# Performance work log

Measured on AMD Instinct MI355X. Metric: run time of the kernel, lower is better.

## Reference

```python
import jax, jax.numpy as jnp
import numpy as np

N = 50000    # nodes
E = 600000   # edges
F = 128      # num_features
ED = 16      # edge_dim
H = 4        # heads
D = 32       # per-head channels = hidden_units // heads
HID = H * D  # hidden_units = 128
C = 10       # num_classes


def _lin(k, fan_in, fan_out):
    # torch.nn.Linear-style init scale
    return jax.random.uniform(k, (fan_in, fan_out), jnp.float32, -1.0, 1.0) / np.sqrt(fan_in)


def setup_inputs() -> dict:
    key = jax.random.key(0)
    ks = jax.random.split(key, 24)
    inp = {
        "x": jax.random.normal(ks[0], (N, F), jnp.float32),
        "edge_index": jax.random.randint(ks[1], (2, E), 0, N, dtype=jnp.int32),
        "edge_attr": jax.random.normal(ks[2], (E, ED), jnp.float32),
    }
    j = 3
    for l, ind in enumerate([F, HID]):
        specs = {"q": (ind, HID, True), "k": (ind, HID, True), "v": (ind, HID, True),
                 "e": (ED, HID, False), "s": (ind, HID, True)}
        for nm, (i, o, bias) in specs.items():
            inp[f"W{nm}{l}"] = _lin(ks[j], i, o); j += 1
            if bias:
                inp[f"b{nm}{l}"] = jnp.zeros((o,), jnp.float32)
    inp["Wout"] = _lin(ks[j], HID, C)
    inp["bout"] = jnp.zeros((C,), jnp.float32)
    return inp


def _transformer_conv(x, src, dst, eattr, Wq, bq, Wk, bk, Wv, bv, We, Ws, bs):
    # PyG TransformerConv: concat=True, root_weight=True, beta=False, eval dropout.
    n = x.shape[0]
    q = (x @ Wq + bq).reshape(n, H, D)
    k = (x @ Wk + bk).reshape(n, H, D)
    v = (x @ Wv + bv).reshape(n, H, D)
    e = (eattr @ We).reshape(-1, H, D)           # edge embedding, added to key and value
    kj = k[src] + e                              # [E, H, D]
    vj = v[src] + e                              # [E, H, D]
    logits = jnp.einsum("ehd,ehd->eh", q[dst], kj) / np.sqrt(D)
    m = jax.ops.segment_max(logits, dst, num_segments=n)          # [N, H]
    ex = jnp.exp(logits - m[dst])
    denom = jax.ops.segment_sum(ex, dst, num_segments=n)          # [N, H]
    alpha = ex / (denom[dst] + 1e-16)                             # PyG softmax eps
    out = jax.ops.segment_sum(vj * alpha[..., None], dst, num_segments=n)
    return out.reshape(n, HID) + x @ Ws + bs                      # concat heads + skip


def reference(x, edge_index, edge_attr,
              Wq0, bq0, Wk0, bk0, Wv0, bv0, We0, Ws0, bs0,
              Wq1, bq1, Wk1, bk1, Wv1, bv1, We1, Ws1, bs1,
              Wout, bout):
    src, dst = edge_index[0], edge_index[1]
    h = jax.nn.relu(_transformer_conv(x, src, dst, edge_attr,
                                      Wq0, bq0, Wk0, bk0, Wv0, bv0, We0, Ws0, bs0))
    h = jax.nn.relu(_transformer_conv(h, src, dst, edge_attr,
                                      Wq1, bq1, Wk1, bk1, Wv1, bv1, We1, Ws1, bs1))
    logits = h @ Wout + bout
    return jax.nn.log_softmax(logits, axis=1)
```

## Files before the change

### kernel.cpp

```cpp
#include <hip/hip_runtime.h>

typedef unsigned short u16;
typedef unsigned int u32;
typedef __attribute__((ext_vector_type(4))) u16 u16x4;
typedef __attribute__((ext_vector_type(8))) u16 u16x8;
typedef __attribute__((ext_vector_type(4))) u32 u32x4;
typedef __attribute__((ext_vector_type(8))) short short8;
typedef __attribute__((ext_vector_type(4))) float f32x4;
typedef __attribute__((ext_vector_type(4))) float f4;

#define NN 50000
#define NE 600000
#define HEADS 4
#define DH 32
#define HIDU 128
#define NC 10
#define NBLK 196
#define WES_T 34
#define WES_H 546

__device__ __forceinline__ float bf2f(u16 u) {
    union { unsigned int i; float f; } c; c.i = ((unsigned int)u) << 16; return c.f;
}
__device__ __forceinline__ u16 f2bf(float f) {
    union { float f; unsigned int i; } c; c.f = f;
    unsigned int x = c.i;
    return (u16)((x + 0x7fffu + ((x >> 16) & 1u)) >> 16);
}
__device__ __forceinline__ float lo_bf(u32 d) { return __uint_as_float(d << 16); }
__device__ __forceinline__ float hi_bf(u32 d) { return __uint_as_float(d & 0xffff0000u); }
__device__ __forceinline__ float qadd_xor1(float v) {
    int o = __builtin_amdgcn_update_dpp(0, __float_as_int(v), 0xB1, 0xF, 0xF, true);
    return v + __int_as_float(o);
}
__device__ __forceinline__ float qadd_xor2(float v) {
    int o = __builtin_amdgcn_update_dpp(0, __float_as_int(v), 0x4E, 0xF, 0xF, true);
    return v + __int_as_float(o);
}

__global__ void k_zero(int* p, int n) {
    int i = blockIdx.x * blockDim.x + threadIdx.x;
    if (i < n) p[i] = 0;
}

__global__ void k_hist(const int* __restrict__ dst, int* __restrict__ deg) {
    int i = blockIdx.x * blockDim.x + threadIdx.x;
    if (i < NE) atomicAdd(&deg[dst[i]], 1);
}

__global__ __launch_bounds__(256) void scan_a(const int* __restrict__ deg,
                                              int* __restrict__ bsum) {
    __shared__ int red[4];
    int i = blockIdx.x * 256 + threadIdx.x;
    int v = (i < NN) ? deg[i] : 0;
    #pragma unroll
    for (int off = 1; off < 64; off <<= 1) v += __shfl_xor(v, off);
    if ((threadIdx.x & 63) == 0) red[threadIdx.x >> 6] = v;
    __syncthreads();
    if (threadIdx.x == 0) bsum[blockIdx.x] = red[0] + red[1] + red[2] + red[3];
}

__global__ __launch_bounds__(256) void scan_b(const int* __restrict__ bsum,
                                              int* __restrict__ boff,
                                              int* __restrict__ row_ptr) {
    __shared__ int s[256];
    int t = threadIdx.x;
    int v = (t < NBLK) ? bsum[t] : 0;
    s[t] = v;
    __syncthreads();
    for (int off = 1; off < 256; off <<= 1) {
        int x = (t >= off) ? s[t - off] : 0;
        __syncthreads();
        s[t] += x;
        __syncthreads();
    }
    if (t < NBLK) boff[t] = s[t] - v;
    if (t == 0) row_ptr[NN] = NE;
}

__global__ __launch_bounds__(256) void scan_c(const int* __restrict__ deg,
                                              const int* __restrict__ boff,
                                              int* __restrict__ row_ptr,
                                              int* __restrict__ cursor) {
    __shared__ int s[256];
    int t = threadIdx.x;
    int i = blockIdx.x * 256 + t;
    int v = (i < NN) ? deg[i] : 0;
    s[t] = v;
    __syncthreads();
    for (int off = 1; off < 256; off <<= 1) {
        int x = (t >= off) ? s[t - off] : 0;
        __syncthreads();
        s[t] += x;
        __syncthreads();
    }
    if (i < NN) {
        int r = boff[blockIdx.x] + s[t] - v;
        row_ptr[i] = r;
        cursor[i] = r;
    }
}

__global__ void k_scatter(const int* __restrict__ ei, const float* __restrict__ eattr,
                          int* __restrict__ cursor,
                          int* __restrict__ csr_src, u16* __restrict__ ea16) {
    int i = blockIdx.x * blockDim.x + threadIdx.x;
    if (i < NE) {
        int s = ei[i];
        int d = ei[NE + i];
        int pos = atomicAdd(&cursor[d], 1);
        csr_src[pos] = s;
        const f4* ep = (const f4*)(eattr + (size_t)i * 16);
        f4 a = ep[0], b = ep[1], c = ep[2], dd = ep[3];
        u16x8 o0, o1;
        #pragma unroll
        for (int j = 0; j < 4; j++) {
            o0[j] = f2bf(a[j]); o0[4 + j] = f2bf(b[j]);
            o1[j] = f2bf(c[j]); o1[4 + j] = f2bf(dd[j]);
        }
        *(u16x8*)(ea16 + (size_t)pos * 16)     = o0;
        *(u16x8*)(ea16 + (size_t)pos * 16 + 8) = o1;
    }
}

__global__ void k_cvtw(const float* w0, const float* w1, const float* w2, const float* w3,
                       const float* w4, const float* w5, const float* w6, const float* w7,
                       u16* __restrict__ hi) {
    const float* w;
    switch (blockIdx.x) {
        case 0: w = w0; break; case 1: w = w1; break;
        case 2: w = w2; break; case 3: w = w3; break;
        case 4: w = w4; break; case 5: w = w5; break;
        case 6: w = w6; break; default: w = w7; break;
    }
    u16* oh = hi + blockIdx.x * 16384;
    for (int i = 0; i < 64; i++) {
        int idx = threadIdx.x + i * 256;
        int k = idx >> 7, n = idx & 127;
        oh[n * 128 + k] = f2bf(w[idx]);
    }
}

__global__ __launch_bounds__(256) void gemm_qkvs(
    const float* __restrict__ X, const u16* __restrict__ WtHi,
    const float* __restrict__ b0, const float* __restrict__ b1,
    const float* __restrict__ b2, const float* __restrict__ b3,
    float* __restrict__ outq, u16* __restrict__ outk, u16* __restrict__ outv,
    float* __restrict__ outs, int nrows)
{
    __shared__ u16 Bs[128 * 128];
    const int mat = blockIdx.y;
    const u16* wh = WtHi + mat * 16384;

    #pragma unroll
    for (int i = 0; i < 8; i++) {
        int idx = threadIdx.x + i * 256;
        int n = idx >> 4, g = idx & 15;
        *(u16x8*)(&Bs[n * 128 + ((g ^ (n & 15)) << 3)]) = *(const u16x8*)(wh + n * 128 + g * 8);
    }
    __syncthreads();

    const int wave = threadIdx.x >> 6, lane = threadIdx.x & 63;
    const int n0 = lane & 15;
    const int qw = lane >> 4;
    const int kq = qw * 8;

    const float* xp[2];
    #pragma unroll
    for (int rt = 0; rt < 2; rt++) {
        int arow = blockIdx.x * 128 + wave * 32 + rt * 16 + n0;
        int arow_c = arow < nrows ? arow : nrows - 1;
        xp[rt] = X + (size_t)arow_c * HIDU + kq;
    }

    f32x4 acc[2][8];
    #pragma unroll
    for (int rt = 0; rt < 2; rt++)
        #pragma unroll
        for (int nt = 0; nt < 8; nt++) acc[rt][nt] = (f32x4){0.f, 0.f, 0.f, 0.f};

    #pragma unroll
    for (int ks = 0; ks < 4; ks++) {
        short8 ah[2];
        #pragma unroll
        for (int rt = 0; rt < 2; rt++) {
            f4 a0 = *(const f4*)(xp[rt] + ks * 32);
            f4 a1 = *(const f4*)(xp[rt] + ks * 32 + 4);
            #pragma unroll
            for (int j = 0; j < 4; j++) {
                ah[rt][j]     = (short)(__float_as_uint(a0[j]) >> 16);
                ah[rt][4 + j] = (short)(__float_as_uint(a1[j]) >> 16);
            }
        }
        #pragma unroll
        for (int nt = 0; nt < 8; nt++) {
            const int boff = (nt * 16 + n0) * 128 + (((ks << 2) + qw) ^ n0) * 8;
            short8 bh = *(const short8*)(&Bs[boff]);
            #pragma unroll
            for (int rt = 0; rt < 2; rt++)
                acc[rt][nt] = __builtin_amdgcn_mfma_f32_16x16x32_bf16(ah[rt], bh, acc[rt][nt], 0, 0, 0);
        }
    }

    const float* bia = (mat == 0) ? b0 : (mat == 1) ? b1 : (mat == 2) ? b2 : b3;
    #pragma unroll
    for (int rt = 0; rt < 2; rt++) {
        const int rbase = blockIdx.x * 128 + wave * 32 + rt * 16 + qw * 4;
        #pragma unroll
        for (int nt = 0; nt < 8; nt++) {
            int col = nt * 16 + n0;
            float bv = bia[col];
            #pragma unroll
            for (int r = 0; r < 4; r++) {
                int grow = rbase + r;
                if (grow < nrows) {
                    float v = acc[rt][nt][r] + bv;
                    if (mat == 0)      outq[(size_t)grow * HIDU + col] = v;
                    else if (mat == 1) outk[(size_t)grow * HIDU + col] = f2bf(v);
                    else if (mat == 2) outv[(size_t)grow * HIDU + col] = f2bf(v);
                    else               outs[(size_t)grow * HIDU + col] = v;
                }
            }
        }
    }
}

__global__ __launch_bounds__(256) void attn(
    const float* __restrict__ qb, const u16* __restrict__ kb, const u16* __restrict__ vb,
    const float* __restrict__ sb, const u16* __restrict__ ea16, const float* __restrict__ We,
    const int* __restrict__ row_ptr, const int* __restrict__ csr_src,
    float* __restrict__ hout_f32,
    const float* __restrict__ Wout, const float* __restrict__ bout,
    float* __restrict__ out_logits, int mode)
{
    __shared__ float WeS[4 * WES_H];
    __shared__ float WoS[HIDU * NC];
    __shared__ float boS[NC];
    __shared__ float hrowS[16 * 132];
    __shared__ float lgS[16 * 16];

    #pragma unroll
    for (int i = 0; i < 8; i++) {
        int idx = threadIdx.x + i * 256;
        int tt = idx >> 7, c = idx & 127;
        int h = c >> 5, j = c & 31;
        WeS[h * WES_H + tt * WES_T + j] = We[idx];
    }
    if (mode == 1) {
        for (int i = 0; i < 5; i++) {
            int idx = threadIdx.x + i * 256;
            if (idx < HIDU * NC) WoS[idx] = Wout[idx];
        }
        if (threadIdx.x < NC) boS[threadIdx.x] = bout[threadIdx.x];
    }
    __syncthreads();

    int gtid = blockIdx.x * 256 + threadIdx.x;
    int n   = gtid >> 4;
    int l16 = gtid & 15;
    int h   = l16 >> 2;
    int sub = l16 & 3;
    const int lane = threadIdx.x & 63;
    const float* WeH = &WeS[h * WES_H];
    const int j0  = sub * 8;
    const int ch0 = h * DH + j0;
    const int t0  = sub * 4;

    f4 qa, qbv;
    float g4[4];
    {
        const f4* qp = (const f4*)(qb + (size_t)n * HIDU + h * DH);
        float q32[32];
        #pragma unroll
        for (int c = 0; c < 8; c++) {
            f4 x = qp[c];
            #pragma unroll
            for (int j = 0; j < 4; j++) q32[c * 4 + j] = x[j];
        }
        #pragma unroll
        for (int tt = 0; tt < 4; tt++) {
            float a = 0.f;
            #pragma unroll
            for (int j = 0; j < 32; j++) a += q32[j] * WeH[(t0 + tt) * WES_T + j];
            g4[tt] = a;
        }
        #pragma unroll
        for (int j = 0; j < 4; j++) { qa[j] = q32[j0 + j]; qbv[j] = q32[j0 + 4 + j]; }
    }

    float m = -INFINITY, l = 0.f;
    f4 O0 = {0.f, 0.f, 0.f, 0.f}, O1 = {0.f, 0.f, 0.f, 0.f};
    f4 a4 = {0.f, 0.f, 0.f, 0.f};

    const int r0 = row_ptr[n], r1 = row_ptr[n + 1];
    const float inv = 0.17677669529663687f;

    for (int e = r0; e < r1; e += 2) {
        bool has2 = (e + 1 < r1);
        int e1i = has2 ? e + 1 : e;
        int s0 = csr_src[e];
        int s1 = csr_src[e1i];
        u16x4 e0 = *(const u16x4*)(ea16 + (size_t)e * 16 + t0);
        u16x4 e1 = *(const u16x4*)(ea16 + (size_t)e1i * 16 + t0);

        u32x4 k0 = *(const u32x4*)(kb + (size_t)s0 * HIDU + ch0);
        u32x4 v0 = *(const u32x4*)(vb + (size_t)s0 * HIDU + ch0);
        u32x4 k1 = *(const u32x4*)(kb + (size_t)s1 * HIDU + ch0);
        u32x4 v1 = *(const u32x4*)(vb + (size_t)s1 * HIDU + ch0);

        f4 k0a = {lo_bf(k0[0]), hi_bf(k0[0]), lo_bf(k0[1]), hi_bf(k0[1])};
        f4 k0b = {lo_bf(k0[2]), hi_bf(k0[2]), lo_bf(k0[3]), hi_bf(k0[3])};
        f4 k1a = {lo_bf(k1[0]), hi_bf(k1[0]), lo_bf(k1[1]), hi_bf(k1[1])};
        f4 k1b = {lo_bf(k1[2]), hi_bf(k1[2]), lo_bf(k1[3]), hi_bf(k1[3])};
        f4 ea0 = {bf2f(e0[0]), bf2f(e0[1]), bf2f(e0[2]), bf2f(e0[3])};
        f4 ea1 = {bf2f(e1[0]), bf2f(e1[1]), bf2f(e1[2]), bf2f(e1[3])};
        f4 g4v = {g4[0], g4[1], g4[2], g4[3]};

        f4 acc0 = qa * k0a + qbv * k0b + g4v * ea0;
        f4 acc1 = qa * k1a + qbv * k1b + g4v * ea1;
        float d0 = acc0[0] + acc0[1] + acc0[2] + acc0[3];
        float d1 = acc1[0] + acc1[1] + acc1[2] + acc1[3];
        d0 = qadd_xor1(d0);  d1 = qadd_xor1(d1);
        d0 = qadd_xor2(d0);  d1 = qadd_xor2(d1);

        float logit0 = d0 * inv;
        float logit1 = has2 ? d1 * inv : -INFINITY;
        float mn = fmaxf(m, fmaxf(logit0, logit1));
        float corr = __expf(m - mn);
        float w0 = __expf(logit0 - mn);
        float w1 = __expf(logit1 - mn);
        l = l * corr + w0 + w1;

        f4 v0a = {lo_bf(v0[0]), hi_bf(v0[0]), lo_bf(v0[1]), hi_bf(v0[1])};
        f4 v0b = {lo_bf(v0[2]), hi_bf(v0[2]), lo_bf(v0[3]), hi_bf(v0[3])};
        f4 v1a = {lo_bf(v1[0]), hi_bf(v1[0]), lo_bf(v1[1]), hi_bf(v1[1])};
        f4 v1b = {lo_bf(v1[2]), hi_bf(v1[2]), lo_bf(v1[3]), hi_bf(v1[3])};
        O0 = O0 * corr + v0a * w0 + v1a * w1;
        O1 = O1 * corr + v0b * w0 + v1b * w1;
        a4 = a4 * corr + ea0 * w0 + ea1 * w1;
        m = mn;
    }

    float af[16];
    #pragma unroll
    for (int t = 0; t < 16; t++)
        af[t] = __shfl(a4[t & 3], (lane & ~3) | (t >> 2));

    float invl = 1.0f / (l + 1e-16f);
    const float* sp = sb + (size_t)n * HIDU + ch0;

    float vals[8];
    #pragma unroll
    for (int j = 0; j < 8; j++) {
        float ev = 0.f;
        #pragma unroll
        for (int t = 0; t < 16; t++) ev += af[t] * WeH[t * WES_T + j0 + j];
        float Oj = (j < 4) ? O0[j] : O1[j - 4];
        vals[j] = fmaxf((Oj + ev) * invl + sp[j], 0.f);
    }

    if (mode == 0) {
        const size_t obase = (size_t)n * HIDU + ch0;
        f4 r0v, r1v;
        #pragma unroll
        for (int j = 0; j < 4; j++) { r0v[j] = vals[j]; r1v[j] = vals[4 + j]; }
        *(f4*)(hout_f32 + obase) = r0v;
        *(f4*)(hout_f32 + obase + 4) = r1v;
    } else {
        const int cb = threadIdx.x >> 4;
        float* hr = &hrowS[cb * 132];
        f4 w0v, w1v;
        #pragma unroll
        for (int j = 0; j < 4; j++) { w0v[j] = vals[j]; w1v[j] = vals[4 + j]; }
        *(f4*)(hr + ch0) = w0v;
        *(f4*)(hr + ch0 + 4) = w1v;
        if (l16 < NC) {
            float lg = boS[l16];
            for (int ch = 0; ch < HIDU; ch += 4) {
                f4 hv = *(const f4*)(hr + ch);
                #pragma unroll
                for (int j = 0; j < 4; j++) lg += hv[j] * WoS[(ch + j) * NC + l16];
            }
            lgS[cb * 16 + l16] = lg;
        }
        if (l16 < NC) {
            float lgc = lgS[cb * 16 + l16];
            float mx = -INFINITY;
            #pragma unroll
            for (int c = 0; c < NC; c++) mx = fmaxf(mx, lgS[cb * 16 + c]);
            float sum = 0.f;
            #pragma unroll
            for (int c = 0; c < NC; c++) sum += __expf(lgS[cb * 16 + c] - mx);
            float lse = mx + __logf(sum);
            out_logits[(size_t)n * NC + l16] = lgc - lse;
        }
    }
}

extern "C" void kernel_launch(void* const* d_in, const int* in_sizes, int n_in,
                              void* d_out, int out_size, void* d_ws, size_t ws_size,
                              hipStream_t stream) {
    const float* x     = (const float*)d_in[0];
    const int*   ei    = (const int*)d_in[1];
    const float* eattr = (const float*)d_in[2];
    const float *Wq0 = (const float*)d_in[3],  *bq0 = (const float*)d_in[4];
    const float *Wk0 = (const float*)d_in[5],  *bk0 = (const float*)d_in[6];
    const float *Wv0 = (const float*)d_in[7],  *bv0 = (const float*)d_in[8];
    const float *We0 = (const float*)d_in[9];
    const float *Ws0 = (const float*)d_in[10], *bs0 = (const float*)d_in[11];
    const float *Wq1 = (const float*)d_in[12], *bq1 = (const float*)d_in[13];
    const float *Wk1 = (const float*)d_in[14], *bk1 = (const float*)d_in[15];
    const float *Wv1 = (const float*)d_in[16], *bv1 = (const float*)d_in[17];
    const float *We1 = (const float*)d_in[18];
    const float *Ws1 = (const float*)d_in[19], *bs1 = (const float*)d_in[20];
    const float *Wout = (const float*)d_in[21], *bout = (const float*)d_in[22];

    char* p = (char*)d_ws;
    auto alloc = [&](size_t bytes) -> void* {
        void* r = (void*)p;
        p += (bytes + 255) & ~(size_t)255;
        return r;
    };
    int* deg      = (int*)alloc(NN * 4);
    int* row_ptr  = (int*)alloc((NN + 1) * 4);
    int* cursor   = (int*)alloc(NN * 4);
    int* bsum     = (int*)alloc(NBLK * 4);
    int* boff     = (int*)alloc(NBLK * 4);
    int* csr_src  = (int*)alloc((size_t)NE * 4);
    float* qb     = (float*)alloc((size_t)NN * HIDU * 4);
    u16* kb       = (u16*)alloc((size_t)NN * HIDU * 2);
    u16* vb       = (u16*)alloc((size_t)NN * HIDU * 2);
    float* sbuf   = (float*)alloc((size_t)NN * HIDU * 4);
    float* hbuf   = (float*)alloc((size_t)NN * HIDU * 4);
    u16* ea16     = (u16*)alloc((size_t)NE * 16 * 2);
    u16* wthi     = (u16*)alloc(8 * 16384 * 2);

    k_zero<<<(NN + 255) / 256, 256, 0, stream>>>(deg, NN);
    k_hist<<<(NE + 255) / 256, 256, 0, stream>>>(ei + NE, deg);
    scan_a<<<NBLK, 256, 0, stream>>>(deg, bsum);
    scan_b<<<1, 256, 0, stream>>>(bsum, boff, row_ptr);
    scan_c<<<NBLK, 256, 0, stream>>>(deg, boff, row_ptr, cursor);
    k_scatter<<<(NE + 255) / 256, 256, 0, stream>>>(ei, eattr, cursor, csr_src, ea16);

    k_cvtw<<<8, 256, 0, stream>>>(Wq0, Wk0, Wv0, Ws0, Wq1, Wk1, Wv1, Ws1, wthi);

    const int gm = (NN + 127) / 128;
    const int ga = (NN * 16) / 256;

    gemm_qkvs<<<dim3(gm, 4), 256, 0, stream>>>(x, wthi, bq0, bk0, bv0, bs0,
                                               qb, kb, vb, sbuf, NN);
    attn<<<ga, 256, 0, stream>>>(qb, kb, vb, sbuf, ea16, We0, row_ptr, csr_src,
                                 hbuf, Wout, bout, (float*)d_out, 0);
    gemm_qkvs<<<dim3(gm, 4), 256, 0, stream>>>(hbuf, wthi + 4 * 16384, bq1, bk1, bv1, bs1,
                                               qb, kb, vb, sbuf, NN);
    attn<<<ga, 256, 0, stream>>>(qb, kb, vb, sbuf, ea16, We1, row_ptr, csr_src,
                                 hbuf, Wout, bout, (float*)d_out, 1);
}
```

Before: 452.8 us.

## Unroll attention edge loop by four, templatize mode, shuffle-reduce output projection

Templates the attention kernel on mode so shared buffers and branches for the unused path vanish. It processes four edges per online-softmax step instead of two, using exp2 with a prescaled logit constant. The q·We projection is now split across the 4 lanes of a head and combined with DPP reductions, replacing a 32-wide per-lane loop. The final classifier is computed by all 16 lanes with a transposed Wout in shared memory and xor-shuffle reductions, removing the LDS staging of hidden rows. More loads in flight per iteration should hide gather latency, at the cost of extra registers and wasted duplicate loads on nodes with few edges.

Result: faster. 433.1 us (-4.4%).

```diff
diff --git a/kernel.cpp b/kernel.cpp
--- a/kernel.cpp
+++ b/kernel.cpp
@@ -8,6 +8,7 @@
 typedef __attribute__((ext_vector_type(8))) short short8;
 typedef __attribute__((ext_vector_type(4))) float f32x4;
 typedef __attribute__((ext_vector_type(4))) float f4;
+typedef __attribute__((ext_vector_type(2))) float f2;
 
 #define NN 50000
 #define NE 600000
@@ -18,6 +19,8 @@
 #define NBLK 196
 #define WES_T 34
 #define WES_H 546
+
+#define SCALE2 0.25503486164f
 
 __device__ __forceinline__ float bf2f(u16 u) {
     union { unsigned int i; float f; } c; c.i = ((unsigned int)u) << 16; return c.f;
@@ -225,19 +228,18 @@
     }
 }
 
-__global__ __launch_bounds__(256) void attn(
+template<int MODE>
+__global__ __launch_bounds__(256) void attn_t(
     const float* __restrict__ qb, const u16* __restrict__ kb, const u16* __restrict__ vb,
     const float* __restrict__ sb, const u16* __restrict__ ea16, const float* __restrict__ We,
     const int* __restrict__ row_ptr, const int* __restrict__ csr_src,
     float* __restrict__ hout_f32,
     const float* __restrict__ Wout, const float* __restrict__ bout,
-    float* __restrict__ out_logits, int mode)
+    float* __restrict__ out_logits)
 {
     __shared__ float WeS[4 * WES_H];
-    __shared__ float WoS[HIDU * NC];
-    __shared__ float boS[NC];
-    __shared__ float hrowS[16 * 132];
-    __shared__ float lgS[16 * 16];
+    __shared__ float WoT[MODE ? (NC * HIDU) : 1];
+    __shared__ float boS[MODE ? NC : 1];
 
     #pragma unroll
     for (int i = 0; i < 8; i++) {
@@ -246,10 +248,14 @@
         int h = c >> 5, j = c & 31;
         WeS[h * WES_H + tt * WES_T + j] = We[idx];
     }
-    if (mode == 1) {
+    if (MODE == 1) {
+        #pragma unroll
         for (int i = 0; i < 5; i++) {
             int idx = threadIdx.x + i * 256;
-            if (idx < HIDU * NC) WoS[idx] = Wout[idx];
+            if (idx < HIDU * NC) {
+                int c = idx >> 7, ch = idx & 127;
+                WoT[idx] = Wout[ch * NC + c];
+            }
         }
         if (threadIdx.x < NC) boS[threadIdx.x] = bout[threadIdx.x];
     }
@@ -267,25 +273,24 @@
     const int t0  = sub * 4;
 
     f4 qa, qbv;
-    float g4[4];
     {
-        const f4* qp = (const f4*)(qb + (size_t)n * HIDU + h * DH);
-        float q32[32];
-        #pragma unroll
-        for (int c = 0; c < 8; c++) {
-            f4 x = qp[c];
-            #pragma unroll
-            for (int j = 0; j < 4; j++) q32[c * 4 + j] = x[j];
-        }
-        #pragma unroll
-        for (int tt = 0; tt < 4; tt++) {
-            float a = 0.f;
-            #pragma unroll
-            for (int j = 0; j < 32; j++) a += q32[j] * WeH[(t0 + tt) * WES_T + j];
-            g4[tt] = a;
-        }
-        #pragma unroll
-        for (int j = 0; j < 4; j++) { qa[j] = q32[j0 + j]; qbv[j] = q32[j0 + 4 + j]; }
+        const f4* qp = (const f4*)(qb + (size_t)n * HIDU + ch0);
+        qa = qp[0]; qbv = qp[1];
+    }
+
+    f4 g4v;
+    {
+        float part[16];
+        #pragma unroll
+        for (int t = 0; t < 16; t++) {
+            const f2* wp = (const f2*)(WeH + t * WES_T + j0);
+            f2 w0 = wp[0], w1 = wp[1], w2 = wp[2], w3 = wp[3];
+            part[t] = qa[0] * w0.x + qa[1] * w0.y + qa[2] * w1.x + qa[3] * w1.y
+                    + qbv[0] * w2.x + qbv[1] * w2.y + qbv[2] * w3.x + qbv[3] * w3.y;
+        }
+        #pragma unroll
+        for (int t = 0; t < 16; t++) { part[t] = qadd_xor1(part[t]); part[t] = qadd_xor2(part[t]); }
+        g4v[0] = part[t0]; g4v[1] = part[t0 + 1]; g4v[2] = part[t0 + 2]; g4v[3] = part[t0 + 3];
     }
 
     float m = -INFINITY, l = 0.f;
@@ -293,51 +298,73 @@
     f4 a4 = {0.f, 0.f, 0.f, 0.f};
 
     const int r0 = row_ptr[n], r1 = row_ptr[n + 1];
-    const float inv = 0.17677669529663687f;
-
-    for (int e = r0; e < r1; e += 2) {
-        bool has2 = (e + 1 < r1);
-        int e1i = has2 ? e + 1 : e;
-        int s0 = csr_src[e];
-        int s1 = csr_src[e1i];
-        u16x4 e0 = *(const u16x4*)(ea16 + (size_t)e * 16 + t0);
-        u16x4 e1 = *(const u16x4*)(ea16 + (size_t)e1i * 16 + t0);
-
+
+    for (int e = r0; e < r1; e += 4) {
+        const int e1 = (e + 1 < r1) ? e + 1 : e;
+        const int e2 = (e + 2 < r1) ? e + 2 : e;
+        const int e3 = (e + 3 < r1) ? e + 3 : e;
+        int s0 = csr_src[e], s1 = csr_src[e1], s2 = csr_src[e2], s3 = csr_src[e3];
+        u16x4 x0 = *(const u16x4*)(ea16 + (size_t)e  * 16 + t0);
+        u16x4 x1 = *(const u16x4*)(ea16 + (size_t)e1 * 16 + t0);
+        u16x4 x2 = *(const u16x4*)(ea16 + (size_t)e2 * 16 + t0);
+        u16x4 x3 = *(const u16x4*)(ea16 + (size_t)e3 * 16 + t0);
         u32x4 k0 = *(const u32x4*)(kb + (size_t)s0 * HIDU + ch0);
+        u32x4 k1 = *(const u32x4*)(kb + (size_t)s1 * HIDU + ch0);
+        u32x4 k2 = *(const u32x4*)(kb + (size_t)s2 * HIDU + ch0);
+        u32x4 k3 = *(const u32x4*)(kb + (size_t)s3 * HIDU + ch0);
         u32x4 v0 = *(const u32x4*)(vb + (size_t)s0 * HIDU + ch0);
-        u32x4 k1 = *(const u32x4*)(kb + (size_t)s1 * HIDU + ch0);
         u32x4 v1 = *(const u32x4*)(vb + (size_t)s1 * HIDU + ch0);
-
-        f4 k0a = {lo_bf(k0[0]), hi_bf(k0[0]), lo_bf(k0[1]), hi_bf(k0[1])};
-        f4 k0b = {lo_bf(k0[2]), hi_bf(k0[2]), lo_bf(k0[3]), hi_bf(k0[3])};
-        f4 k1a = {lo_bf(k1[0]), hi_bf(k1[0]), lo_bf(k1[1]), hi_bf(k1[1])};
-        f4 k1b = {lo_bf(k1[2]), hi_bf(k1[2]), lo_bf(k1[3]), hi_bf(k1[3])};
-        f4 ea0 = {bf2f(e0[0]), bf2f(e0[1]), bf2f(e0[2]), bf2f(e0[3])};
-        f4 ea1 = {bf2f(e1[0]), bf2f(e1[1]), bf2f(e1[2]), bf2f(e1[3])};
-        f4 g4v = {g4[0], g4[1], g4[2], g4[3]};
-
-        f4 acc0 = qa * k0a + qbv * k0b + g4v * ea0;
-        f4 acc1 = qa * k1a + qbv * k1b + g4v * ea1;
-        float d0 = acc0[0] + acc0[1] + acc0[2] + acc0[3];
-        float d1 = acc1[0] + acc1[1] + acc1[2] + acc1[3];
-        d0 = qadd_xor1(d0);  d1 = qadd_xor1(d1);
-        d0 = qadd_xor2(d0);  d1 = qadd_xor2(d1);
-
-        float logit0 = d0 * inv;
-        float logit1 = has2 ? d1 * inv : -INFINITY;
-        float mn = fmaxf(m, fmaxf(logit0, logit1));
-        float corr = __expf(m - mn);
-        float w0 = __expf(logit0 - mn);
-        float w1 = __expf(logit1 - mn);
-        l = l * corr + w0 + w1;
-
-        f4 v0a = {lo_bf(v0[0]), hi_bf(v0[0]), lo_bf(v0[1]), hi_bf(v0[1])};
-        f4 v0b = {lo_bf(v0[2]), hi_bf(v0[2]), lo_bf(v0[3]), hi_bf(v0[3])};
-        f4 v1a = {lo_bf(v1[0]), hi_bf(v1[0]), lo_bf(v1[1]), hi_bf(v1[1])};
-        f4 v1b = {lo_bf(v1[2]), hi_bf(v1[2]), lo_bf(v1[3]), hi_bf(v1[3])};
-        O0 = O0 * corr + v0a * w0 + v1a * w1;
-        O1 = O1 * corr + v0b * w0 + v1b * w1;
-        a4 = a4 * corr + ea0 * w0 + ea1 * w1;
+        u32x4 v2 = *(const u32x4*)(vb + (size_t)s2 * HIDU + ch0);
+        u32x4 v3 = *(const u32x4*)(vb + (size_t)s3 * HIDU + ch0);
+
+        f4 ea0 = {bf2f(x0[0]), bf2f(x0[1]), bf2f(x0[2]), bf2f(x0[3])};
+        f4 ea1 = {bf2f(x1[0]), bf2f(x1[1]), bf2f(x1[2]), bf2f(x1[3])};
+        f4 ea2 = {bf2f(x2[0]), bf2f(x2[1]), bf2f(x2[2]), bf2f(x2[3])};
+        f4 ea3 = {bf2f(x3[0]), bf2f(x3[1]), bf2f(x3[2]), bf2f(x3[3])};
+
+        f4 ac0 = qa * (f4){lo_bf(k0[0]), hi_bf(k0[0]), lo_bf(k0[1]), hi_bf(k0[1])}
+               + qbv * (f4){lo_bf(k0[2]), hi_bf(k0[2]), lo_bf(k0[3]), hi_bf(k0[3])}
+               + g4v * ea0;
+        f4 ac1 = qa * (f4){lo_bf(k1[0]), hi_bf(k1[0]), lo_bf(k1[1]), hi_bf(k1[1])}
+               + qbv * (f4){lo_bf(k1[2]), hi_bf(k1[2]), lo_bf(k1[3]), hi_bf(k1[3])}
+               + g4v * ea1;
+        f4 ac2 = qa * (f4){lo_bf(k2[0]), hi_bf(k2[0]), lo_bf(k2[1]), hi_bf(k2[1])}
+               + qbv * (f4){lo_bf(k2[2]), hi_bf(k2[2]), lo_bf(k2[3]), hi_bf(k2[3])}
+               + g4v * ea2;
+        f4 ac3 = qa * (f4){lo_bf(k3[0]), hi_bf(k3[0]), lo_bf(k3[1]), hi_bf(k3[1])}
+               + qbv * (f4){lo_bf(k3[2]), hi_bf(k3[2]), lo_bf(k3[3]), hi_bf(k3[3])}
+               + g4v * ea3;
+        float d0 = (ac0[0] + ac0[1]) + (ac0[2] + ac0[3]);
+        float d1 = (ac1[0] + ac1[1]) + (ac1[2] + ac1[3]);
+        float d2 = (ac2[0] + ac2[1]) + (ac2[2] + ac2[3]);
+        float d3 = (ac3[0] + ac3[1]) + (ac3[2] + ac3[3]);
+        d0 = qadd_xor1(d0); d1 = qadd_xor1(d1); d2 = qadd_xor1(d2); d3 = qadd_xor1(d3);
+        d0 = qadd_xor2(d0); d1 = qadd_xor2(d1); d2 = qadd_xor2(d2); d3 = qadd_xor2(d3);
+
+        float lg0 = d0 * SCALE2;
+        float lg1 = (e + 1 < r1) ? d1 * SCALE2 : -INFINITY;
+        float lg2 = (e + 2 < r1) ? d2 * SCALE2 : -INFINITY;
+        float lg3 = (e + 3 < r1) ? d3 * SCALE2 : -INFINITY;
+        float pm = fmaxf(fmaxf(lg0, lg1), fmaxf(lg2, lg3));
+        float mn = fmaxf(m, pm);
+        float corr = exp2f(m - mn);
+        float w0 = exp2f(lg0 - mn);
+        float w1 = exp2f(lg1 - mn);
+        float w2 = exp2f(lg2 - mn);
+        float w3 = exp2f(lg3 - mn);
+        l = l * corr + ((w0 + w1) + (w2 + w3));
+
+        O0 = O0 * corr
+           + (f4){lo_bf(v0[0]), hi_bf(v0[0]), lo_bf(v0[1]), hi_bf(v0[1])} * w0
+           + (f4){lo_bf(v1[0]), hi_bf(v1[0]), lo_bf(v1[1]), hi_bf(v1[1])} * w1
+           + (f4){lo_bf(v2[0]), hi_bf(v2[0]), lo_bf(v2[1]), hi_bf(v2[1])} * w2
+           + (f4){lo_bf(v3[0]), hi_bf(v3[0]), lo_bf(v3[1]), hi_bf(v3[1])} * w3;
+        O1 = O1 * corr
+           + (f4){lo_bf(v0[2]), hi_bf(v0[2]), lo_bf(v0[3]), hi_bf(v0[3])} * w0
+           + (f4){lo_bf(v1[2]), hi_bf(v1[2]), lo_bf(v1[3]), hi_bf(v1[3])} * w1
+           + (f4){lo_bf(v2[2]), hi_bf(v2[2]), lo_bf(v2[3]), hi_bf(v2[3])} * w2
+           + (f4){lo_bf(v3[2]), hi_bf(v3[2]), lo_bf(v3[3]), hi_bf(v3[3])} * w3;
+        a4 = a4 * corr + ea0 * w0 + ea1 * w1 + ea2 * w2 + ea3 * w3;
         m = mn;
     }
 
@@ -349,51 +376,50 @@
     float invl = 1.0f / (l + 1e-16f);
     const float* sp = sb + (size_t)n * HIDU + ch0;
 
-    float vals[8];
-    #pragma unroll
-    for (int j = 0; j < 8; j++) {
-        float ev = 0.f;
-        #pragma unroll
-        for (int t = 0; t < 16; t++) ev += af[t] * WeH[t * WES_T + j0 + j];
-        float Oj = (j < 4) ? O0[j] : O1[j - 4];
-        vals[j] = fmaxf((Oj + ev) * invl + sp[j], 0.f);
-    }
-
-    if (mode == 0) {
+    f4 evA = {0.f, 0.f, 0.f, 0.f}, evB = {0.f, 0.f, 0.f, 0.f};
+    #pragma unroll
+    for (int t = 0; t < 16; t++) {
+        float a = af[t];
+        const f2* wp = (const f2*)(WeH + t * WES_T + j0);
+        f2 w0 = wp[0], w1 = wp[1], w2 = wp[2], w3 = wp[3];
+        evA[0] += a * w0.x; evA[1] += a * w0.y; evA[2] += a * w1.x; evA[3] += a * w1.y;
+        evB[0] += a * w2.x; evB[1] += a * w2.y; evB[2] += a * w3.x; evB[3] += a * w3.y;
+    }
+
+    f4 val0, val1;
+    #pragma unroll
+    for (int j = 0; j < 4; j++) {
+        val0[j] = fmaxf((O0[j] + evA[j]) * invl + sp[j], 0.f);
+        val1[j] = fmaxf((O1[j] + evB[j]) * invl + sp[4 + j], 0.f);
+    }
+
+    if (MODE == 0) {
         const size_t obase = (size_t)n * HIDU + ch0;
-        f4 r0v, r1v;
-        #pragma unroll
-        for (int j = 0; j < 4; j++) { r0v[j] = vals[j]; r1v[j] = vals[4 + j]; }
-        *(f4*)(hout_f32 + obase) = r0v;
-        *(f4*)(hout_f32 + obase + 4) = r1v;
+        *(f4*)(hout_f32 + obase) = val0;
+        *(f4*)(hout_f32 + obase + 4) = val1;
     } else {
-        const int cb = threadIdx.x >> 4;
-        float* hr = &hrowS[cb * 132];
-        f4 w0v, w1v;
-        #pragma unroll
-        for (int j = 0; j < 4; j++) { w0v[j] = vals[j]; w1v[j] = vals[4 + j]; }
-        *(f4*)(hr + ch0) = w0v;
-        *(f4*)(hr + ch0 + 4) = w1v;
-        if (l16 < NC) {
-            float lg = boS[l16];
-            for (int ch = 0; ch < HIDU; ch += 4) {
-                f4 hv = *(const f4*)(hr + ch);
-                #pragma unroll
-                for (int j = 0; j < 4; j++) lg += hv[j] * WoS[(ch + j) * NC + l16];
-            }
-            lgS[cb * 16 + l16] = lg;
-        }
-        if (l16 < NC) {
-            float lgc = lgS[cb * 16 + l16];
-            float mx = -INFINITY;
+        float plg[NC];
+        #pragma unroll
+        for (int c = 0; c < NC; c++) {
+            const f4* wr = (const f4*)(WoT + c * HIDU + ch0);
+            f4 wa = wr[0], wb = wr[1];
+            plg[c] = val0[0] * wa[0] + val0[1] * wa[1] + val0[2] * wa[2] + val0[3] * wa[3]
+                   + val1[0] * wb[0] + val1[1] * wb[1] + val1[2] * wb[2] + val1[3] * wb[3];
+        }
+        #pragma unroll
+        for (int mask = 1; mask < 16; mask <<= 1) {
             #pragma unroll
-            for (int c = 0; c < NC; c++) mx = fmaxf(mx, lgS[cb * 16 + c]);
-            float sum = 0.f;
-            #pragma unroll
-            for (int c = 0; c < NC; c++) sum += __expf(lgS[cb * 16 + c] - mx);
-            float lse = mx + __logf(sum);
-            out_logits[(size_t)n * NC + l16] = lgc - lse;
-        }
+            for (int c = 0; c < NC; c++) plg[c] += __shfl_xor(plg[c], mask);
+        }
+        float lg[NC];
+        float mx = -INFINITY;
+        #pragma unroll
+        for (int c = 0; c < NC; c++) { lg[c] = plg[c] + boS[c]; mx = fmaxf(mx, lg[c]); }
+        float sum = 0.f;
+        #pragma unroll
+        for (int c = 0; c < NC; c++) sum += __expf(lg[c] - mx);
+        float lse = mx + __logf(sum);
+        if (l16 < NC) out_logits[(size_t)n * NC + l16] = lg[l16] - lse;
     }
 }
 
@@ -449,10 +475,10 @@
 
     gemm_qkvs<<<dim3(gm, 4), 256, 0, stream>>>(x, wthi, bq0, bk0, bv0, bs0,
                                                qb, kb, vb, sbuf, NN);
-    attn<<<ga, 256, 0, stream>>>(qb, kb, vb, sbuf, ea16, We0, row_ptr, csr_src,
-                                 hbuf, Wout, bout, (float*)d_out, 0);
+    attn_t<0><<<ga, 256, 0, stream>>>(qb, kb, vb, sbuf, ea16, We0, row_ptr, csr_src,
+                                      hbuf, nullptr, nullptr, nullptr);
     gemm_qkvs<<<dim3(gm, 4), 256, 0, stream>>>(hbuf, wthi + 4 * 16384, bq1, bk1, bv1, bs1,
                                                qb, kb, vb, sbuf, NN);
-    attn<<<ga, 256, 0, stream>>>(qb, kb, vb, sbuf, ea16, We1, row_ptr, csr_src,
-                                 hbuf, Wout, bout, (float*)d_out, 1);
-}
+    attn_t<1><<<ga, 256, 0, stream>>>(qb, kb, vb, sbuf, ea16, We1, row_ptr, csr_src,
+                                      nullptr, Wout, bout, (float*)d_out);
+}
```
